# Kernel tuning notes

Measured on AMD Instinct MI355X. Metric: run time of the kernel, lower is better.

## Reference

```python
import jax, jax.numpy as jnp
import numpy as np

HEADS = 8


def setup_inputs() -> dict:
    key = jax.random.key(0)
    ks = jax.random.split(key, 9)
    B, C, H, W = 16, 512, 32, 32
    d = C // HEADS
    scale = d ** -0.5
    return {
        "x": jax.random.normal(ks[0], (B, C, H, W), dtype=jnp.float32),
        "Wq": jax.random.normal(ks[1], (C, C), dtype=jnp.float32) * (C ** -0.5),
        "bq": jax.random.normal(ks[2], (C,), dtype=jnp.float32) * 0.02,
        "Wk": jax.random.normal(ks[3], (C, C), dtype=jnp.float32) * (C ** -0.5),
        "bk": jax.random.normal(ks[4], (C,), dtype=jnp.float32) * 0.02,
        "Wv": jax.random.normal(ks[5], (C, C), dtype=jnp.float32) * (C ** -0.5),
        "bv": jax.random.normal(ks[6], (C,), dtype=jnp.float32) * 0.02,
        "rel_h": jax.random.normal(ks[7], (d, H, 1), dtype=jnp.float32) * scale,
        "rel_w": jax.random.normal(ks[8], (d, 1, W), dtype=jnp.float32) * scale,
    }


def reference(x, Wq, bq, Wk, bk, Wv, bv, rel_h, rel_w):
    B, C, H, W = x.shape
    heads = HEADS
    d = C // heads
    scale = d ** -0.5
    N = H * W
    xf = x.reshape(B, C, N)  # 1x1 conv == per-pixel linear over channels
    q = (jnp.einsum('oc,bcn->bon', Wq, xf) + bq[:, None]).reshape(B, heads, d, N)
    k = (jnp.einsum('oc,bcn->bon', Wk, xf) + bk[:, None]).reshape(B, heads, d, N)
    v = (jnp.einsum('oc,bcn->bon', Wv, xf) + bv[:, None]).reshape(B, heads, d, N)
    q = q * scale
    # content-content scores [B, heads, N, N]
    cc = jnp.einsum('bhdi,bhdj->bhij', q, k)
    # relative position bias table [d, N], projected by q
    cp_tab = (rel_h + rel_w).reshape(d, N)
    cp = jnp.einsum('bhdi,dj->bhij', q, cp_tab)
    beta = jax.nn.softmax(cc + cp, axis=-1)
    attn = jnp.einsum('bhij,bhdj->bhid', beta, v)  # [B, heads, N, d]
    # original does .view(x.shape) on [b,h,i,d] -> keep same raw reshape
    return attn.reshape(B, C, H, W)
```

## Files before the change

kernel.cpp:

```cpp
#include <hip/hip_runtime.h>
#include <hip/hip_bf16.h>
#include <stdint.h>

typedef unsigned short u16;
typedef u16 u16x8 __attribute__((ext_vector_type(8)));
typedef u16 u16x4 __attribute__((ext_vector_type(4)));
typedef __bf16 bf16x8 __attribute__((ext_vector_type(8)));
typedef float f32x4 __attribute__((ext_vector_type(4)));

#define MFMA16(a, b, c) __builtin_amdgcn_mfma_f32_16x16x32_bf16((a), (b), (c), 0, 0, 0)

#define SCALE_Q 0.18033688011112042f

__device__ __forceinline__ u16 f2b(float f) {
    union { float f; unsigned u; } v; v.f = f;
    unsigned r = v.u + 0x7FFFu + ((v.u >> 16) & 1u);
    return (u16)(r >> 16);
}
__device__ __forceinline__ u16 f2b_h(float f) {
    union { float f; unsigned u; } v; v.f = f;
    return (u16)((v.u + 0x8000u) >> 16);
}

__global__ __launch_bounds__(256) void wconv(const float* __restrict__ Wq,
                                             const float* __restrict__ Wk,
                                             const float* __restrict__ Wv,
                                             u16* __restrict__ wb) {
    int g = blockIdx.x * 256 + threadIdx.x;
    int which = g >> 15;
    const float* src = which == 0 ? Wq : (which == 1 ? Wk : Wv);
    int off = (g & 32767) * 8;
    f32x4 a = *(const f32x4*)(src + off);
    f32x4 b = *(const f32x4*)(src + off + 4);
    u16x8 o;
#pragma unroll
    for (int i = 0; i < 4; ++i) { o[i] = f2b_h(a[i]); o[4 + i] = f2b_h(b[i]); }
    *(u16x8*)(wb + (size_t)g * 8) = o;
}

__global__ __launch_bounds__(256) void qkv_proj(
    const float* __restrict__ x, const u16* __restrict__ wb,
    const float* __restrict__ bq, const float* __restrict__ bk,
    const float* __restrict__ bv,
    const float* __restrict__ rel_h, const float* __restrict__ rel_w,
    u16* __restrict__ qws, u16* __restrict__ kws, u16* __restrict__ vws) {
    __shared__ __align__(16) u16 Xs[128 * 72];
    __shared__ __align__(16) u16 Ws[128 * 72];

    const int tid  = threadIdx.x;
    const int wave = tid >> 6, lane = tid & 63;
    const int quad = lane >> 4, l16 = lane & 15;
    const int wr = wave >> 1, wc = wave & 1;

    const int id = blockIdx.x;
    const int nt = id & 7;
    const int r  = id >> 3;
    const int o0 = r & 3;
    const int r2 = r >> 2;
    const int mm = r2 % 3;
    const int b  = r2 / 3;
    const int N0 = nt * 128;
    const int O0 = o0 * 128;

    const u16*   W    = wb + (size_t)mm * 262144;
    const float* bias = mm == 0 ? bq : (mm == 1 ? bk : bv);
    const float* xb   = x + ((size_t)b << 19);

    f32x4 acc[4][4] = {};

    for (int kt = 0; kt < 8; ++kt) {
        __syncthreads();
#pragma unroll
        for (int rep = 0; rep < 4; ++rep) {
            int id2 = tid + rep * 256;
            int oct = id2 >> 7;
            int n   = id2 & 127;
            const float* xp = xb + (size_t)(kt * 64 + oct * 8) * 1024 + N0 + n;
            u16x8 xv;
#pragma unroll
            for (int k = 0; k < 8; ++k) xv[k] = f2b_h(xp[k * 1024]);
            *(u16x8*)(Xs + n * 72 + oct * 8) = xv;
            int row = id2 >> 3, c8 = id2 & 7;
            *(u16x8*)(Ws + row * 72 + c8 * 8) =
                *(const u16x8*)(W + ((size_t)(O0 + row) << 9) + kt * 64 + c8 * 8);
        }
        __syncthreads();
#pragma unroll
        for (int kk = 0; kk < 2; ++kk) {
            bf16x8 af[4], bfr[4];
#pragma unroll
            for (int mi = 0; mi < 4; ++mi)
                af[mi] = *(bf16x8*)(Xs + (wr * 64 + mi * 16 + l16) * 72 + kk * 32 + quad * 8);
#pragma unroll
            for (int ni = 0; ni < 4; ++ni)
                bfr[ni] = *(bf16x8*)(Ws + (wc * 64 + ni * 16 + l16) * 72 + kk * 32 + quad * 8);
#pragma unroll
            for (int mi = 0; mi < 4; ++mi)
#pragma unroll
                for (int ni = 0; ni < 4; ++ni)
                    acc[mi][ni] = MFMA16(af[mi], bfr[ni], acc[mi][ni]);
        }
    }

#pragma unroll
    for (int mi = 0; mi < 4; ++mi) {
#pragma unroll
        for (int ni = 0; ni < 4; ++ni) {
            int o  = O0 + wc * 64 + ni * 16 + l16;
            int h  = o >> 6, dd = o & 63;
            size_t bh = (size_t)b * 8 + h;
            float bv_ = bias[o];
            int n0 = N0 + wr * 64 + mi * 16 + quad * 4;
            if (mm == 2) {
                u16x4 pk;
#pragma unroll
                for (int rr = 0; rr < 4; ++rr) pk[rr] = f2b(acc[mi][ni][rr] + bv_);
                *(u16x4*)(vws + (bh * 64 + dd) * 1024 + n0) = pk;
            } else if (mm == 0) {
#pragma unroll
                for (int rr = 0; rr < 4; ++rr)
                    qws[(bh * 1024 + (n0 + rr)) * 64 + dd] =
                        f2b((acc[mi][ni][rr] + bv_) * SCALE_Q);
            } else {
                float th = rel_h[dd * 32 + (n0 >> 5)];
                f32x4 tw = *(const f32x4*)(rel_w + dd * 32 + (n0 & 31));
#pragma unroll
                for (int rr = 0; rr < 4; ++rr)
                    kws[(bh * 1024 + n0 + rr) * 64 + dd] =
                        f2b(acc[mi][ni][rr] + bv_ + th + tw[rr]);
            }
        }
    }
}

__global__ __launch_bounds__(256, 4) void attn(
    const u16* __restrict__ qws, const u16* __restrict__ kws,
    const u16* __restrict__ vws, float* __restrict__ out) {
    __shared__ __align__(16) u16 KP[64 * 72];
    __shared__ __align__(16) u16 Vt[64 * 72];
    __shared__ __align__(16) u16 Pb[4 * 32 * 68];

    const int tid  = threadIdx.x;
    const int wave = tid >> 6, lane = tid & 63;
    const int quad = lane >> 4, l16 = lane & 15;
    const int id = blockIdx.x;
    const int h  = id & 7;
    const int qt = (id >> 3) & 7;
    const int b  = id >> 6;
    const size_t bh = (size_t)b * 8 + h;

    const u16* Q = qws + (bh * 1024 + (size_t)qt * 128) * 64;
    const u16* K = kws + bh * 1024 * 64;
    const u16* V = vws + bh * 64 * 1024;

    const int srow = tid >> 3, sc8 = tid & 7;

    bf16x8 qf[2][2];
#pragma unroll
    for (int ni = 0; ni < 2; ++ni)
#pragma unroll
        for (int ks = 0; ks < 2; ++ks)
            qf[ni][ks] = *(const bf16x8*)(Q + (wave * 32 + ni * 16 + l16) * 64 + ks * 32 + quad * 8);

    f32x4 accO[4][2] = {};
    f32x4 s4[2] = {};
    u16* Pw = Pb + wave * 2176;

    u16x8 kr0, kr1, vr0, vr1;
    kr0 = *(const u16x8*)(K + (size_t)srow * 64 + sc8 * 8);
    kr1 = *(const u16x8*)(K + (size_t)(srow + 32) * 64 + sc8 * 8);
    vr0 = *(const u16x8*)(V + ((size_t)srow << 10) + sc8 * 8);
    vr1 = *(const u16x8*)(V + ((size_t)(srow + 32) << 10) + sc8 * 8);

    for (int jt = 0; jt < 16; ++jt) {
        __syncthreads();
        *(u16x8*)(KP + srow * 72 + sc8 * 8)        = kr0;
        *(u16x8*)(KP + (srow + 32) * 72 + sc8 * 8) = kr1;
        *(u16x8*)(Vt + srow * 72 + sc8 * 8)        = vr0;
        *(u16x8*)(Vt + (srow + 32) * 72 + sc8 * 8) = vr1;
        __syncthreads();

        if (jt < 15) {
            const u16* Kn = K + (size_t)(jt + 1) * 64 * 64;
            const u16* Vn = V + (size_t)(jt + 1) * 64;
            kr0 = *(const u16x8*)(Kn + (size_t)srow * 64 + sc8 * 8);
            kr1 = *(const u16x8*)(Kn + (size_t)(srow + 32) * 64 + sc8 * 8);
            vr0 = *(const u16x8*)(Vn + ((size_t)srow << 10) + sc8 * 8);
            vr1 = *(const u16x8*)(Vn + ((size_t)(srow + 32) << 10) + sc8 * 8);
        }

        f32x4 accST[4][2] = {};
#pragma unroll
        for (int ks = 0; ks < 2; ++ks) {
            bf16x8 kf[4];
#pragma unroll
            for (int mj = 0; mj < 4; ++mj)
                kf[mj] = *(bf16x8*)(KP + (mj * 16 + l16) * 72 + ks * 32 + quad * 8);
#pragma unroll
            for (int mj = 0; mj < 4; ++mj)
#pragma unroll
                for (int ni = 0; ni < 2; ++ni)
                    accST[mj][ni] = MFMA16(kf[mj], qf[ni][ks], accST[mj][ni]);
        }
#pragma unroll
        for (int ni = 0; ni < 2; ++ni)
#pragma unroll
            for (int mj = 0; mj < 4; ++mj) {
                f32x4 p;
#pragma unroll
                for (int rr = 0; rr < 4; ++rr)
                    p[rr] = __builtin_amdgcn_exp2f(accST[mj][ni][rr]);
                s4[ni] += p;
                u16x4 pk;
#pragma unroll
                for (int rr = 0; rr < 4; ++rr) pk[rr] = f2b_h(p[rr]);
                *(u16x4*)(Pw + (ni * 16 + l16) * 68 + mj * 16 + quad * 4) = pk;
            }
#pragma unroll
        for (int ks2 = 0; ks2 < 2; ++ks2) {
            bf16x8 vf[4], pf[2];
#pragma unroll
            for (int md = 0; md < 4; ++md)
                vf[md] = *(bf16x8*)(Vt + (md * 16 + l16) * 72 + ks2 * 32 + quad * 8);
#pragma unroll
            for (int ni = 0; ni < 2; ++ni)
                pf[ni] = *(bf16x8*)(Pw + (ni * 16 + l16) * 68 + ks2 * 32 + quad * 8);
#pragma unroll
            for (int md = 0; md < 4; ++md)
#pragma unroll
                for (int ni = 0; ni < 2; ++ni)
                    accO[md][ni] = MFMA16(vf[md], pf[ni], accO[md][ni]);
        }
    }

#pragma unroll
    for (int ni = 0; ni < 2; ++ni) {
        float rs = (s4[ni][0] + s4[ni][1]) + (s4[ni][2] + s4[ni][3]);
        rs += __shfl_xor(rs, 16);
        rs += __shfl_xor(rs, 32);
        float inv = 1.0f / rs;
        int i = qt * 128 + wave * 32 + ni * 16 + l16;
#pragma unroll
        for (int md = 0; md < 4; ++md) {
            f32x4 pk;
#pragma unroll
            for (int rr = 0; rr < 4; ++rr) pk[rr] = accO[md][ni][rr] * inv;
            int dd = md * 16 + quad * 4;
            *(f32x4*)(out + (bh * 1024 + i) * 64 + dd) = pk;
        }
    }
}

extern "C" void kernel_launch(void* const* d_in, const int* in_sizes, int n_in,
                              void* d_out, int out_size, void* d_ws, size_t ws_size,
                              hipStream_t stream) {
    const float* x  = (const float*)d_in[0];
    const float* Wq = (const float*)d_in[1];
    const float* bq = (const float*)d_in[2];
    const float* Wk = (const float*)d_in[3];
    const float* bk = (const float*)d_in[4];
    const float* Wv = (const float*)d_in[5];
    const float* bv = (const float*)d_in[6];
    const float* rh = (const float*)d_in[7];
    const float* rw = (const float*)d_in[8];
    float* out = (float*)d_out;

    u16* kws = (u16*)d_ws;
    u16* vws = kws + 8388608;
    u16* qws = vws + 8388608;
    u16* wb  = qws + 8388608;

    wconv<<<384, 256, 0, stream>>>(Wq, Wk, Wv, wb);
    qkv_proj<<<1536, 256, 0, stream>>>(x, wb, bq, bk, bv, rh, rw, qws, kws, vws);
    attn<<<1024, 256, 0, stream>>>(qws, kws, vws, out);
}
```

Measured before the change: 216.5 us.

## Pre-transpose x to bf16 and register-prefetch tiles in QKV projection

Merges the weight conversion with a new pass that converts x to bf16 and transposes it to pixel-major layout, staging it in the output buffer as scratch. The projection kernel then loads contiguous 16-byte bf16 rows for both operands and prefetches the next k-tile into registers while the MFMAs run. This replaces the repeated strided fp32 loads and per-element conversions that were done once per output tile (12 times per x element). In exchange it adds an extra read and write of x and depends on the output buffer being free until the attention kernel overwrites it.

New measurement: 202.9 us. -6.3%, faster.

```diff
diff --git a/kernel.cpp b/kernel.cpp
--- a/kernel.cpp
+++ b/kernel.cpp
@@ -22,24 +22,57 @@
     return (u16)((v.u + 0x8000u) >> 16);
 }
 
-__global__ __launch_bounds__(256) void wconv(const float* __restrict__ Wq,
-                                             const float* __restrict__ Wk,
-                                             const float* __restrict__ Wv,
-                                             u16* __restrict__ wb) {
-    int g = blockIdx.x * 256 + threadIdx.x;
-    int which = g >> 15;
-    const float* src = which == 0 ? Wq : (which == 1 ? Wk : Wv);
-    int off = (g & 32767) * 8;
-    f32x4 a = *(const f32x4*)(src + off);
-    f32x4 b = *(const f32x4*)(src + off + 4);
-    u16x8 o;
-#pragma unroll
-    for (int i = 0; i < 4; ++i) { o[i] = f2b_h(a[i]); o[4 + i] = f2b_h(b[i]); }
-    *(u16x8*)(wb + (size_t)g * 8) = o;
-}
-
-__global__ __launch_bounds__(256) void qkv_proj(
-    const float* __restrict__ x, const u16* __restrict__ wb,
+__global__ __launch_bounds__(256) void prep(
+    const float* __restrict__ x,
+    const float* __restrict__ Wq, const float* __restrict__ Wk,
+    const float* __restrict__ Wv,
+    u16* __restrict__ wb, u16* __restrict__ xT) {
+    __shared__ __align__(16) u16 Ls[128 * 72];
+    const int tid = threadIdx.x;
+
+    if (blockIdx.x < 384) {
+        int g = blockIdx.x * 256 + tid;
+        int which = g >> 15;
+        const float* src = which == 0 ? Wq : (which == 1 ? Wk : Wv);
+        int off = (g & 32767) * 8;
+        f32x4 a = *(const f32x4*)(src + off);
+        f32x4 b = *(const f32x4*)(src + off + 4);
+        u16x8 o;
+#pragma unroll
+        for (int i = 0; i < 4; ++i) { o[i] = f2b_h(a[i]); o[4 + i] = f2b_h(b[i]); }
+        *(u16x8*)(wb + (size_t)g * 8) = o;
+        return;
+    }
+
+    const int bid = blockIdx.x - 384;
+    const int b  = bid >> 6;
+    const int ct = (bid >> 3) & 7;
+    const int nt = bid & 7;
+    const int C0 = ct * 64, N0 = nt * 128;
+    const float* xb = x + ((size_t)b << 19);
+
+#pragma unroll
+    for (int rep = 0; rep < 4; ++rep) {
+        int id = tid + rep * 256;
+        int oct = id >> 7, n = id & 127;
+        const float* xp = xb + (size_t)(C0 + oct * 8) * 1024 + N0 + n;
+        u16x8 xv;
+#pragma unroll
+        for (int k = 0; k < 8; ++k) xv[k] = f2b_h(xp[k * 1024]);
+        *(u16x8*)(Ls + n * 72 + oct * 8) = xv;
+    }
+    __syncthreads();
+#pragma unroll
+    for (int rep = 0; rep < 4; ++rep) {
+        int id = tid + rep * 256;
+        int n = id >> 3, c8 = id & 7;
+        *(u16x8*)(xT + ((size_t)b << 19) + (size_t)(N0 + n) * 512 + C0 + c8 * 8) =
+            *(u16x8*)(Ls + n * 72 + c8 * 8);
+    }
+}
+
+__global__ __launch_bounds__(256, 3) void qkv_proj(
+    const u16* __restrict__ xT, const u16* __restrict__ wb,
     const float* __restrict__ bq, const float* __restrict__ bk,
     const float* __restrict__ bv,
     const float* __restrict__ rel_h, const float* __restrict__ rel_w,
@@ -64,27 +97,35 @@
 
     const u16*   W    = wb + (size_t)mm * 262144;
     const float* bias = mm == 0 ? bq : (mm == 1 ? bk : bv);
-    const float* xb   = x + ((size_t)b << 19);
+    const u16*   Xb   = xT + ((size_t)b << 19);
+
+    const int sr = tid >> 3, sc8 = tid & 7;
+
+    u16x8 xr[4], wrg[4];
+#pragma unroll
+    for (int rp = 0; rp < 4; ++rp) {
+        xr[rp]  = *(const u16x8*)(Xb + (size_t)(N0 + sr + rp * 32) * 512 + sc8 * 8);
+        wrg[rp] = *(const u16x8*)(W  + (size_t)(O0 + sr + rp * 32) * 512 + sc8 * 8);
+    }
 
     f32x4 acc[4][4] = {};
 
     for (int kt = 0; kt < 8; ++kt) {
         __syncthreads();
 #pragma unroll
-        for (int rep = 0; rep < 4; ++rep) {
-            int id2 = tid + rep * 256;
-            int oct = id2 >> 7;
-            int n   = id2 & 127;
-            const float* xp = xb + (size_t)(kt * 64 + oct * 8) * 1024 + N0 + n;
-            u16x8 xv;
-#pragma unroll
-            for (int k = 0; k < 8; ++k) xv[k] = f2b_h(xp[k * 1024]);
-            *(u16x8*)(Xs + n * 72 + oct * 8) = xv;
-            int row = id2 >> 3, c8 = id2 & 7;
-            *(u16x8*)(Ws + row * 72 + c8 * 8) =
-                *(const u16x8*)(W + ((size_t)(O0 + row) << 9) + kt * 64 + c8 * 8);
+        for (int rp = 0; rp < 4; ++rp) {
+            *(u16x8*)(Xs + (sr + rp * 32) * 72 + sc8 * 8) = xr[rp];
+            *(u16x8*)(Ws + (sr + rp * 32) * 72 + sc8 * 8) = wrg[rp];
         }
         __syncthreads();
+        if (kt < 7) {
+            int c0 = (kt + 1) * 64;
+#pragma unroll
+            for (int rp = 0; rp < 4; ++rp) {
+                xr[rp]  = *(const u16x8*)(Xb + (size_t)(N0 + sr + rp * 32) * 512 + c0 + sc8 * 8);
+                wrg[rp] = *(const u16x8*)(W  + (size_t)(O0 + sr + rp * 32) * 512 + c0 + sc8 * 8);
+            }
+        }
 #pragma unroll
         for (int kk = 0; kk < 2; ++kk) {
             bf16x8 af[4], bfr[4];
@@ -269,8 +310,9 @@
     u16* vws = kws + 8388608;
     u16* qws = vws + 8388608;
     u16* wb  = qws + 8388608;
-
-    wconv<<<384, 256, 0, stream>>>(Wq, Wk, Wv, wb);
-    qkv_proj<<<1536, 256, 0, stream>>>(x, wb, bq, bk, bv, rh, rw, qws, kws, vws);
+    u16* xT  = (u16*)d_out;
+
+    prep<<<1408, 256, 0, stream>>>(x, Wq, Wk, Wv, wb, xT);
+    qkv_proj<<<1536, 256, 0, stream>>>(xT, wb, bq, bk, bv, rh, rw, qws, kws, vws);
     attn<<<1024, 256, 0, stream>>>(qws, kws, vws, out);
 }
```
